# Optimization experiments

Hardware: AMD Instinct MI355X
Metric: run time of the kernel (lower is better)

## Reference

```python
import jax, jax.numpy as jnp
import numpy as np

EPS = 1e-12  # matches torch.nn.functional.normalize default eps

def _l2_normalize(x):
    # F.normalize: x / max(||x||_2, eps)
    n = jnp.linalg.norm(x, axis=-1, keepdims=True)
    return x / jnp.maximum(n, EPS)

def setup_inputs() -> dict:
    key = jax.random.key(0)
    k_z, k_e = jax.random.split(key)
    B, N, D, K = 8, 4096, 64, 8192
    z = jax.random.normal(k_z, (B, N, D), dtype=jnp.float32)
    # nn.Embedding weight initialized uniform(-1/K, 1/K)
    embedding = jax.random.uniform(k_e, (K, D), dtype=jnp.float32,
                                   minval=-1.0 / K, maxval=1.0 / K)
    return {"z": z, "embedding": embedding, "temperature": 1.0}

def reference(z, embedding, temperature):
    z_norm = _l2_normalize(z)                      # (B,N,D)
    codebook = _l2_normalize(embedding)            # (K,D)
    sim = jnp.einsum('bnd,kd->bnk', z_norm, codebook)  # (B,N,K)
    dists = 1.0 - sim
    probs = jax.nn.softmax(-dists / temperature, axis=-1)  # (B,N,K)
    z_q = jnp.einsum('bnk,kd->bnd', probs, codebook)       # (B,N,D)
    return (probs, z_q)
```

## Files before the change

### kernel.cpp

```cpp
#include <hip/hip_runtime.h>


#define M_TOTAL 32768
#define KCODES  8192
#define DDIM    64
#define KSPLIT  4
#define KCHUNK  (KCODES / KSPLIT)
#define M_ROWS  128

typedef __attribute__((ext_vector_type(8))) short bf16x8;
typedef __attribute__((ext_vector_type(4))) short bf16x4;
typedef __attribute__((ext_vector_type(4))) float f32x4;

__device__ inline unsigned short f2bf(float x) {
  union { float f; unsigned u; } v; v.f = x;
  unsigned r = v.u + 0x7FFFu + ((v.u >> 16) & 1u);
  return (unsigned short)(r >> 16);
}

__global__ __launch_bounds__(256) void norm_rows_kernel(
    const float* __restrict__ in, unsigned short* __restrict__ F,
    unsigned short* __restrict__ FT, int nrows) {
  int row = blockIdx.x * 4 + (threadIdx.x >> 6);
  int d = threadIdx.x & 63;
  if (row >= nrows) return;
  float x = in[(size_t)row * DDIM + d];
  float s = x * x;
  s += __shfl_xor(s, 1);  s += __shfl_xor(s, 2);  s += __shfl_xor(s, 4);
  s += __shfl_xor(s, 8);  s += __shfl_xor(s, 16); s += __shfl_xor(s, 32);
  float scale = 1.0f / fmaxf(sqrtf(s), 1e-12f);
  unsigned short b = f2bf(x * scale);
  {
    int blk = row >> 4, ml = row & 15;
    int h = d >> 5, g = (d >> 3) & 3, j = d & 7;
    F[((size_t)(blk * 2 + h)) * 512 + (g * 16 + ml) * 8 + j] = b;
  }
  if (FT) {
    int ds = d >> 4, dl = d & 15;
    int kb = row >> 5, kg = (row >> 3) & 3, kj = row & 7;
    FT[((size_t)(kb * 4 + ds)) * 512 + (kg * 16 + dl) * 8 + kj] = b;
  }
}

__global__ __launch_bounds__(512, 4) void passA_kernel(
    const unsigned short* __restrict__ FZn,
    const unsigned short* __restrict__ FCb,
    const unsigned short* __restrict__ FCbT,
    const float* __restrict__ tptr,
    float* __restrict__ Up,
    float* __restrict__ rsp) {
  __shared__ __align__(16) unsigned short sbuf[2][4096];
  __shared__ __align__(16) unsigned short etile[8][16 * 56];
  const int tid = threadIdx.x;
  const int w  = tid >> 6, l = tid & 63, g = l >> 4, ml = l & 15;
  const int rb = blockIdx.x & 255;
  const int ks = blockIdx.x >> 8;
  const int m_base = rb * M_ROWS + w * 16;
  const int k0 = ks * KCHUNK;
  const float sc = 1.4426950408889634f / tptr[0];

  const unsigned short* fz = FZn + ((size_t)((rb * 8 + w) * 2)) * 512;
  const bf16x8 zn0 = *(const bf16x8*)(fz + l * 8);
  const bf16x8 zn1 = *(const bf16x8*)(fz + 512 + l * 8);

  const f32x4 zero = {0.f, 0.f, 0.f, 0.f};
  f32x4 uacc[4] = {zero, zero, zero, zero};
  float rs = 0.f;

  const unsigned short* gb = (tid < 256 ? FCb : FCbT) + (size_t)(tid & 255) * 8;
  bf16x8 stg = *(const bf16x8*)(gb + (size_t)k0 * 64);
  int cur = 0;

  const int NIT = KCHUNK / 32;
  for (int it = 0; it < NIT; ++it) {
    *(bf16x8*)&sbuf[cur][tid * 8] = stg;
    if (it + 1 < NIT)
      stg = *(const bf16x8*)(gb + (size_t)(k0 + (it + 1) * 32) * 64);
    __syncthreads();
    const unsigned short* sb = &sbuf[cur][0];
#pragma unroll
    for (int cs = 0; cs < 2; ++cs) {
      const bf16x8 cb0 = *(const bf16x8*)(sb + (cs * 2 + 0) * 512 + l * 8);
      const bf16x8 cb1 = *(const bf16x8*)(sb + (cs * 2 + 1) * 512 + l * 8);
      f32x4 acc = __builtin_amdgcn_mfma_f32_16x16x32_bf16(cb0, zn0, zero, 0, 0, 0);
      acc = __builtin_amdgcn_mfma_f32_16x16x32_bf16(cb1, zn1, acc, 0, 0, 0);
      bf16x4 ep;
#pragma unroll
      for (int r = 0; r < 4; ++r) {
        float e = exp2f((acc[r] - 1.0f) * sc);
        rs += e;
        ep[r] = (short)f2bf(e);
      }
      *(bf16x4*)&etile[w][ml * 56 + cs * 16 + g * 4] = ep;
    }
    asm volatile("s_waitcnt lgkmcnt(0)" ::: "memory");
    const bf16x8 ef = *(const bf16x8*)&etile[w][ml * 56 + g * 8];
#pragma unroll
    for (int ds = 0; ds < 4; ++ds) {
      const bf16x8 ct = *(const bf16x8*)(sb + 2048 + ds * 512 + l * 8);
      uacc[ds] = __builtin_amdgcn_mfma_f32_16x16x32_bf16(ct, ef, uacc[ds], 0, 0, 0);
    }
    cur ^= 1;
  }

  rs += __shfl_xor(rs, 16);
  rs += __shfl_xor(rs, 32);
  if (g == 0) rsp[(size_t)ks * M_TOTAL + m_base + ml] = rs;

  float* urow = Up + ((size_t)ks * M_TOTAL + m_base + ml) * DDIM;
#pragma unroll
  for (int ds = 0; ds < 4; ++ds)
    *(f32x4*)(urow + ds * 16 + g * 4) = uacc[ds];
}

__global__ __launch_bounds__(256) void rs_kernel(
    const float* __restrict__ rsp, float* __restrict__ rs) {
  int m = blockIdx.x * 256 + threadIdx.x;
  float s = 0.f;
#pragma unroll
  for (int ks = 0; ks < KSPLIT; ++ks) s += rsp[(size_t)ks * M_TOTAL + m];
  rs[m] = s;
}

__global__ __launch_bounds__(256) void zq_kernel(
    const float* __restrict__ Up, const float* __restrict__ rs,
    float* __restrict__ zq) {
  size_t i = (size_t)blockIdx.x * 256 + threadIdx.x;
  f32x4 u = *(const f32x4*)(Up + i * 4);
#pragma unroll
  for (int ks = 1; ks < KSPLIT; ++ks) {
    f32x4 p = *(const f32x4*)(Up + (size_t)ks * M_TOTAL * DDIM + i * 4);
#pragma unroll
    for (int r = 0; r < 4; ++r) u[r] += p[r];
  }
  float inv = 1.0f / rs[(i * 4) >> 6];
  f32x4 v = {u[0] * inv, u[1] * inv, u[2] * inv, u[3] * inv};
  *(f32x4*)(zq + i * 4) = v;
}

__global__ __launch_bounds__(512, 4) void probs_kernel(
    const unsigned short* __restrict__ FZn,
    const unsigned short* __restrict__ FCb,
    const float* __restrict__ tptr,
    const float* __restrict__ rsv,
    float* __restrict__ probs) {
  __shared__ __align__(16) unsigned short sbuf[2][4096];
  const int tid = threadIdx.x;
  const int w  = tid >> 6, l = tid & 63, g = l >> 4, ml = l & 15;
  const int rb = blockIdx.x & 255;
  const int ks = blockIdx.x >> 8;
  const int m_base = rb * M_ROWS + w * 16;
  const int k0 = ks * KCHUNK;
  const float sc = 1.4426950408889634f / tptr[0];

  const unsigned short* fz = FZn + ((size_t)((rb * 8 + w) * 2)) * 512;
  const bf16x8 zn0 = *(const bf16x8*)(fz + l * 8);
  const bf16x8 zn1 = *(const bf16x8*)(fz + 512 + l * 8);
  const float inv = 1.0f / rsv[m_base + ml];
  const f32x4 zero = {0.f, 0.f, 0.f, 0.f};
  float* prow = probs + (size_t)(m_base + ml) * KCODES;

  const unsigned short* gb = FCb + (size_t)tid * 8;
  bf16x8 stg = *(const bf16x8*)(gb + (size_t)k0 * 64);
  int cur = 0;

  const int NIT = KCHUNK / 64;
  for (int it = 0; it < NIT; ++it) {
    *(bf16x8*)&sbuf[cur][tid * 8] = stg;
    if (it + 1 < NIT)
      stg = *(const bf16x8*)(gb + (size_t)(k0 + (it + 1) * 64) * 64);
    __syncthreads();
    const unsigned short* sb = &sbuf[cur][0];
    const int kc = k0 + it * 64;
#pragma unroll
    for (int cb = 0; cb < 4; ++cb) {
      const bf16x8 c0 = *(const bf16x8*)(sb + (cb * 2 + 0) * 512 + l * 8);
      const bf16x8 c1 = *(const bf16x8*)(sb + (cb * 2 + 1) * 512 + l * 8);
      f32x4 a = __builtin_amdgcn_mfma_f32_16x16x32_bf16(c0, zn0, zero, 0, 0, 0);
      a = __builtin_amdgcn_mfma_f32_16x16x32_bf16(c1, zn1, a, 0, 0, 0);
      f32x4 p;
#pragma unroll
      for (int r = 0; r < 4; ++r) p[r] = exp2f((a[r] - 1.0f) * sc) * inv;
      *(f32x4*)(prow + kc + cb * 16 + g * 4) = p;
    }
    cur ^= 1;
  }
}

extern "C" void kernel_launch(void* const* d_in, const int* in_sizes, int n_in,
                              void* d_out, int out_size, void* d_ws, size_t ws_size,
                              hipStream_t stream) {
  const float* z    = (const float*)d_in[0];
  const float* emb  = (const float*)d_in[1];
  const float* temp = (const float*)d_in[2];

  float* probs = (float*)d_out;
  float* zq    = probs + (size_t)M_TOTAL * KCODES;

  unsigned short* FZn  = (unsigned short*)d_ws;
  unsigned short* FCb  = FZn + (size_t)M_TOTAL * DDIM;
  unsigned short* FCbT = FCb + (size_t)KCODES * DDIM;
  float* Up  = (float*)(FCbT + (size_t)KCODES * DDIM);
  float* rsp = Up + (size_t)KSPLIT * M_TOTAL * DDIM;
  float* rs  = rsp + (size_t)KSPLIT * M_TOTAL;

  norm_rows_kernel<<<M_TOTAL / 4, 256, 0, stream>>>(z, FZn, nullptr, M_TOTAL);
  norm_rows_kernel<<<KCODES / 4, 256, 0, stream>>>(emb, FCb, FCbT, KCODES);
  passA_kernel<<<256 * KSPLIT, 512, 0, stream>>>(FZn, FCb, FCbT, temp, Up, rsp);
  rs_kernel<<<M_TOTAL / 256, 256, 0, stream>>>(rsp, rs);
  zq_kernel<<<(M_TOTAL * DDIM / 4) / 256, 256, 0, stream>>>(Up, rs, zq);
  probs_kernel<<<256 * KSPLIT, 512, 0, stream>>>(FZn, FCb, temp, rs, probs);
}
```

Measured before the change: 378.1 us.

## Drop LDS staging of codebook, read from global; shrink blocks; fuse rs/zq kernels

The pass-A and probs kernels no longer stage codebook tiles through double-buffered shared memory with block barriers. Each wave now reads codebook fragments directly from global memory (relying on L2/L1 caching), and blocks shrink from 512 to 256 threads with twice as many blocks. The row-sum reduction is folded into the z_q normalization kernel, which removes one launch. bf16 packing now uses the HIP intrinsic conversion. The trade-off is more redundant global/cache traffic per wave in exchange for removing barriers and LDS pressure.

```diff
diff --git a/kernel.cpp b/kernel.cpp
--- a/kernel.cpp
+++ b/kernel.cpp
@@ -1,4 +1,5 @@
 #include <hip/hip_runtime.h>
+#include <hip/hip_bf16.h>
 
 
 #define M_TOTAL 32768
@@ -6,10 +7,8 @@
 #define DDIM    64
 #define KSPLIT  4
 #define KCHUNK  (KCODES / KSPLIT)
-#define M_ROWS  128
 
 typedef __attribute__((ext_vector_type(8))) short bf16x8;
-typedef __attribute__((ext_vector_type(4))) short bf16x4;
 typedef __attribute__((ext_vector_type(4))) float f32x4;
 
 __device__ inline unsigned short f2bf(float x) {
@@ -42,24 +41,23 @@
   }
 }
 
-__global__ __launch_bounds__(512, 4) void passA_kernel(
+__global__ __launch_bounds__(256) void passA_kernel(
     const unsigned short* __restrict__ FZn,
     const unsigned short* __restrict__ FCb,
     const unsigned short* __restrict__ FCbT,
     const float* __restrict__ tptr,
     float* __restrict__ Up,
     float* __restrict__ rsp) {
-  __shared__ __align__(16) unsigned short sbuf[2][4096];
-  __shared__ __align__(16) unsigned short etile[8][16 * 56];
+  __shared__ __align__(16) unsigned short etile[4][16 * 56];
   const int tid = threadIdx.x;
   const int w  = tid >> 6, l = tid & 63, g = l >> 4, ml = l & 15;
-  const int rb = blockIdx.x & 255;
-  const int ks = blockIdx.x >> 8;
-  const int m_base = rb * M_ROWS + w * 16;
+  const int rb = blockIdx.x & 511;
+  const int ks = blockIdx.x >> 9;
+  const int m_base = rb * 64 + w * 16;
   const int k0 = ks * KCHUNK;
   const float sc = 1.4426950408889634f / tptr[0];
 
-  const unsigned short* fz = FZn + ((size_t)((rb * 8 + w) * 2)) * 512;
+  const unsigned short* fz = FZn + ((size_t)((rb * 4 + w) * 2)) * 512;
   const bf16x8 zn0 = *(const bf16x8*)(fz + l * 8);
   const bf16x8 zn1 = *(const bf16x8*)(fz + 512 + l * 8);
 
@@ -67,40 +65,32 @@
   f32x4 uacc[4] = {zero, zero, zero, zero};
   float rs = 0.f;
 
-  const unsigned short* gb = (tid < 256 ? FCb : FCbT) + (size_t)(tid & 255) * 8;
-  bf16x8 stg = *(const bf16x8*)(gb + (size_t)k0 * 64);
-  int cur = 0;
-
-  const int NIT = KCHUNK / 32;
-  for (int it = 0; it < NIT; ++it) {
-    *(bf16x8*)&sbuf[cur][tid * 8] = stg;
-    if (it + 1 < NIT)
-      stg = *(const bf16x8*)(gb + (size_t)(k0 + (it + 1) * 32) * 64);
-    __syncthreads();
-    const unsigned short* sb = &sbuf[cur][0];
+  for (int kc = k0; kc < k0 + KCHUNK; kc += 32) {
+    const unsigned short* fc = FCb + (size_t)(kc >> 4) * 1024;
+    const unsigned short* ft = FCbT + (size_t)(kc >> 5) * 2048;
 #pragma unroll
     for (int cs = 0; cs < 2; ++cs) {
-      const bf16x8 cb0 = *(const bf16x8*)(sb + (cs * 2 + 0) * 512 + l * 8);
-      const bf16x8 cb1 = *(const bf16x8*)(sb + (cs * 2 + 1) * 512 + l * 8);
-      f32x4 acc = __builtin_amdgcn_mfma_f32_16x16x32_bf16(cb0, zn0, zero, 0, 0, 0);
-      acc = __builtin_amdgcn_mfma_f32_16x16x32_bf16(cb1, zn1, acc, 0, 0, 0);
-      bf16x4 ep;
-#pragma unroll
-      for (int r = 0; r < 4; ++r) {
-        float e = exp2f((acc[r] - 1.0f) * sc);
-        rs += e;
-        ep[r] = (short)f2bf(e);
-      }
-      *(bf16x4*)&etile[w][ml * 56 + cs * 16 + g * 4] = ep;
+      const bf16x8 c0 = *(const bf16x8*)(fc + cs * 1024 + l * 8);
+      const bf16x8 c1 = *(const bf16x8*)(fc + cs * 1024 + 512 + l * 8);
+      f32x4 acc = __builtin_amdgcn_mfma_f32_16x16x32_bf16(c0, zn0, zero, 0, 0, 0);
+      acc = __builtin_amdgcn_mfma_f32_16x16x32_bf16(c1, zn1, acc, 0, 0, 0);
+      float e0 = exp2f((acc[0] - 1.0f) * sc);
+      float e1 = exp2f((acc[1] - 1.0f) * sc);
+      float e2 = exp2f((acc[2] - 1.0f) * sc);
+      float e3 = exp2f((acc[3] - 1.0f) * sc);
+      rs += (e0 + e1) + (e2 + e3);
+      union { __hip_bfloat162 h[2]; uint2 u; } pk;
+      pk.h[0] = __float22bfloat162_rn(make_float2(e0, e1));
+      pk.h[1] = __float22bfloat162_rn(make_float2(e2, e3));
+      *(uint2*)&etile[w][ml * 56 + cs * 16 + g * 4] = pk.u;
     }
     asm volatile("s_waitcnt lgkmcnt(0)" ::: "memory");
     const bf16x8 ef = *(const bf16x8*)&etile[w][ml * 56 + g * 8];
 #pragma unroll
     for (int ds = 0; ds < 4; ++ds) {
-      const bf16x8 ct = *(const bf16x8*)(sb + 2048 + ds * 512 + l * 8);
+      const bf16x8 ct = *(const bf16x8*)(ft + ds * 512 + l * 8);
       uacc[ds] = __builtin_amdgcn_mfma_f32_16x16x32_bf16(ct, ef, uacc[ds], 0, 0, 0);
     }
-    cur ^= 1;
   }
 
   rs += __shfl_xor(rs, 16);
@@ -113,19 +103,13 @@
     *(f32x4*)(urow + ds * 16 + g * 4) = uacc[ds];
 }
 
-__global__ __launch_bounds__(256) void rs_kernel(
-    const float* __restrict__ rsp, float* __restrict__ rs) {
-  int m = blockIdx.x * 256 + threadIdx.x;
-  float s = 0.f;
-#pragma unroll
-  for (int ks = 0; ks < KSPLIT; ++ks) s += rsp[(size_t)ks * M_TOTAL + m];
-  rs[m] = s;
-}
-
-__global__ __launch_bounds__(256) void zq_kernel(
-    const float* __restrict__ Up, const float* __restrict__ rs,
-    float* __restrict__ zq) {
+__global__ __launch_bounds__(256) void rszq_kernel(
+    const float* __restrict__ Up, const float* __restrict__ rsp,
+    float* __restrict__ rs, float* __restrict__ zq) {
   size_t i = (size_t)blockIdx.x * 256 + threadIdx.x;
+  int m = (int)(i >> 4);
+  float s = rsp[m] + rsp[M_TOTAL + m] + rsp[2 * M_TOTAL + m] + rsp[3 * M_TOTAL + m];
+  if ((i & 15) == 0) rs[m] = s;
   f32x4 u = *(const f32x4*)(Up + i * 4);
 #pragma unroll
   for (int ks = 1; ks < KSPLIT; ++ks) {
@@ -133,57 +117,45 @@
 #pragma unroll
     for (int r = 0; r < 4; ++r) u[r] += p[r];
   }
-  float inv = 1.0f / rs[(i * 4) >> 6];
+  float inv = 1.0f / s;
   f32x4 v = {u[0] * inv, u[1] * inv, u[2] * inv, u[3] * inv};
   *(f32x4*)(zq + i * 4) = v;
 }
 
-__global__ __launch_bounds__(512, 4) void probs_kernel(
+__global__ __launch_bounds__(256) void probs_kernel(
     const unsigned short* __restrict__ FZn,
     const unsigned short* __restrict__ FCb,
     const float* __restrict__ tptr,
     const float* __restrict__ rsv,
     float* __restrict__ probs) {
-  __shared__ __align__(16) unsigned short sbuf[2][4096];
   const int tid = threadIdx.x;
   const int w  = tid >> 6, l = tid & 63, g = l >> 4, ml = l & 15;
-  const int rb = blockIdx.x & 255;
-  const int ks = blockIdx.x >> 8;
-  const int m_base = rb * M_ROWS + w * 16;
+  const int rb = blockIdx.x & 511;
+  const int ks = blockIdx.x >> 9;
+  const int m_base = rb * 64 + w * 16;
   const int k0 = ks * KCHUNK;
   const float sc = 1.4426950408889634f / tptr[0];
 
-  const unsigned short* fz = FZn + ((size_t)((rb * 8 + w) * 2)) * 512;
+  const unsigned short* fz = FZn + ((size_t)((rb * 4 + w) * 2)) * 512;
   const bf16x8 zn0 = *(const bf16x8*)(fz + l * 8);
   const bf16x8 zn1 = *(const bf16x8*)(fz + 512 + l * 8);
   const float inv = 1.0f / rsv[m_base + ml];
   const f32x4 zero = {0.f, 0.f, 0.f, 0.f};
   float* prow = probs + (size_t)(m_base + ml) * KCODES;
 
-  const unsigned short* gb = FCb + (size_t)tid * 8;
-  bf16x8 stg = *(const bf16x8*)(gb + (size_t)k0 * 64);
-  int cur = 0;
-
-  const int NIT = KCHUNK / 64;
-  for (int it = 0; it < NIT; ++it) {
-    *(bf16x8*)&sbuf[cur][tid * 8] = stg;
-    if (it + 1 < NIT)
-      stg = *(const bf16x8*)(gb + (size_t)(k0 + (it + 1) * 64) * 64);
-    __syncthreads();
-    const unsigned short* sb = &sbuf[cur][0];
-    const int kc = k0 + it * 64;
+  for (int kc = k0; kc < k0 + KCHUNK; kc += 32) {
+    const unsigned short* fc = FCb + (size_t)(kc >> 4) * 1024;
 #pragma unroll
-    for (int cb = 0; cb < 4; ++cb) {
-      const bf16x8 c0 = *(const bf16x8*)(sb + (cb * 2 + 0) * 512 + l * 8);
-      const bf16x8 c1 = *(const bf16x8*)(sb + (cb * 2 + 1) * 512 + l * 8);
+    for (int cs = 0; cs < 2; ++cs) {
+      const bf16x8 c0 = *(const bf16x8*)(fc + cs * 1024 + l * 8);
+      const bf16x8 c1 = *(const bf16x8*)(fc + cs * 1024 + 512 + l * 8);
       f32x4 a = __builtin_amdgcn_mfma_f32_16x16x32_bf16(c0, zn0, zero, 0, 0, 0);
       a = __builtin_amdgcn_mfma_f32_16x16x32_bf16(c1, zn1, a, 0, 0, 0);
       f32x4 p;
 #pragma unroll
       for (int r = 0; r < 4; ++r) p[r] = exp2f((a[r] - 1.0f) * sc) * inv;
-      *(f32x4*)(prow + kc + cb * 16 + g * 4) = p;
+      *(f32x4*)(prow + kc + cs * 16 + g * 4) = p;
     }
-    cur ^= 1;
   }
 }
 
@@ -206,8 +178,7 @@
 
   norm_rows_kernel<<<M_TOTAL / 4, 256, 0, stream>>>(z, FZn, nullptr, M_TOTAL);
   norm_rows_kernel<<<KCODES / 4, 256, 0, stream>>>(emb, FCb, FCbT, KCODES);
-  passA_kernel<<<256 * KSPLIT, 512, 0, stream>>>(FZn, FCb, FCbT, temp, Up, rsp);
-  rs_kernel<<<M_TOTAL / 256, 256, 0, stream>>>(rsp, rs);
-  zq_kernel<<<(M_TOTAL * DDIM / 4) / 256, 256, 0, stream>>>(Up, rs, zq);
-  probs_kernel<<<256 * KSPLIT, 512, 0, stream>>>(FZn, FCb, temp, rs, probs);
+  passA_kernel<<<512 * KSPLIT, 256, 0, stream>>>(FZn, FCb, FCbT, temp, Up, rsp);
+  rszq_kernel<<<(M_TOTAL * DDIM / 4) / 256, 256, 0, stream>>>(Up, rsp, rs, zq);
+  probs_kernel<<<512 * KSPLIT, 256, 0, stream>>>(FZn, FCb, temp, rs, probs);
 }
```

After: 502.0 us. 1.33x slower.

## Process two row tiles per wave in passA and fuse rowsum into zq kernel

Applied to the files above, without the earlier changes.

Each wave in passA now handles 32 rows (two 16-row tiles) instead of 16, so every codebook fragment loaded from shared memory feeds twice as many MFMAs. The grid shrinks to 512 blocks. The rs_kernel and zq_kernel are merged into one kernel that sums the split rowsum partials inline, removing a launch and a round trip through rs. The bf16 packing now uses the packed hip_bf16 conversions. The cost is higher register pressure and fewer blocks in passA, which may hurt occupancy and load balance.

```diff
diff --git a/kernel.cpp b/kernel.cpp
--- a/kernel.cpp
+++ b/kernel.cpp
@@ -1,4 +1,5 @@
 #include <hip/hip_runtime.h>
+#include <hip/hip_bf16.h>
 
 
 #define M_TOTAL 32768
@@ -6,10 +7,8 @@
 #define DDIM    64
 #define KSPLIT  4
 #define KCHUNK  (KCODES / KSPLIT)
-#define M_ROWS  128
 
 typedef __attribute__((ext_vector_type(8))) short bf16x8;
-typedef __attribute__((ext_vector_type(4))) short bf16x4;
 typedef __attribute__((ext_vector_type(4))) float f32x4;
 
 __device__ inline unsigned short f2bf(float x) {
@@ -50,22 +49,26 @@
     float* __restrict__ Up,
     float* __restrict__ rsp) {
   __shared__ __align__(16) unsigned short sbuf[2][4096];
-  __shared__ __align__(16) unsigned short etile[8][16 * 56];
+  __shared__ __align__(16) unsigned short etile[8][2][16 * 56];
   const int tid = threadIdx.x;
   const int w  = tid >> 6, l = tid & 63, g = l >> 4, ml = l & 15;
-  const int rb = blockIdx.x & 255;
-  const int ks = blockIdx.x >> 8;
-  const int m_base = rb * M_ROWS + w * 16;
+  const int rb = blockIdx.x & 127;
+  const int ks = blockIdx.x >> 7;
+  const int mA = rb * 256 + w * 32;
+  const int mB = mA + 16;
   const int k0 = ks * KCHUNK;
   const float sc = 1.4426950408889634f / tptr[0];
 
-  const unsigned short* fz = FZn + ((size_t)((rb * 8 + w) * 2)) * 512;
-  const bf16x8 zn0 = *(const bf16x8*)(fz + l * 8);
-  const bf16x8 zn1 = *(const bf16x8*)(fz + 512 + l * 8);
+  const unsigned short* fz = FZn + ((size_t)((rb * 16 + w * 2) * 2)) * 512;
+  const bf16x8 zA0 = *(const bf16x8*)(fz + l * 8);
+  const bf16x8 zA1 = *(const bf16x8*)(fz + 512 + l * 8);
+  const bf16x8 zB0 = *(const bf16x8*)(fz + 1024 + l * 8);
+  const bf16x8 zB1 = *(const bf16x8*)(fz + 1536 + l * 8);
 
   const f32x4 zero = {0.f, 0.f, 0.f, 0.f};
-  f32x4 uacc[4] = {zero, zero, zero, zero};
-  float rs = 0.f;
+  f32x4 uaccA[4] = {zero, zero, zero, zero};
+  f32x4 uaccB[4] = {zero, zero, zero, zero};
+  float rsA = 0.f, rsB = 0.f;
 
   const unsigned short* gb = (tid < 256 ? FCb : FCbT) + (size_t)(tid & 255) * 8;
   bf16x8 stg = *(const bf16x8*)(gb + (size_t)k0 * 64);
@@ -80,52 +83,61 @@
     const unsigned short* sb = &sbuf[cur][0];
 #pragma unroll
     for (int cs = 0; cs < 2; ++cs) {
-      const bf16x8 cb0 = *(const bf16x8*)(sb + (cs * 2 + 0) * 512 + l * 8);
-      const bf16x8 cb1 = *(const bf16x8*)(sb + (cs * 2 + 1) * 512 + l * 8);
-      f32x4 acc = __builtin_amdgcn_mfma_f32_16x16x32_bf16(cb0, zn0, zero, 0, 0, 0);
-      acc = __builtin_amdgcn_mfma_f32_16x16x32_bf16(cb1, zn1, acc, 0, 0, 0);
-      bf16x4 ep;
-#pragma unroll
-      for (int r = 0; r < 4; ++r) {
-        float e = exp2f((acc[r] - 1.0f) * sc);
-        rs += e;
-        ep[r] = (short)f2bf(e);
-      }
-      *(bf16x4*)&etile[w][ml * 56 + cs * 16 + g * 4] = ep;
+      const bf16x8 c0 = *(const bf16x8*)(sb + cs * 1024 + l * 8);
+      const bf16x8 c1 = *(const bf16x8*)(sb + cs * 1024 + 512 + l * 8);
+      f32x4 aA = __builtin_amdgcn_mfma_f32_16x16x32_bf16(c0, zA0, zero, 0, 0, 0);
+      aA = __builtin_amdgcn_mfma_f32_16x16x32_bf16(c1, zA1, aA, 0, 0, 0);
+      f32x4 aB = __builtin_amdgcn_mfma_f32_16x16x32_bf16(c0, zB0, zero, 0, 0, 0);
+      aB = __builtin_amdgcn_mfma_f32_16x16x32_bf16(c1, zB1, aB, 0, 0, 0);
+      float eA0 = exp2f((aA[0] - 1.0f) * sc), eA1 = exp2f((aA[1] - 1.0f) * sc);
+      float eA2 = exp2f((aA[2] - 1.0f) * sc), eA3 = exp2f((aA[3] - 1.0f) * sc);
+      float eB0 = exp2f((aB[0] - 1.0f) * sc), eB1 = exp2f((aB[1] - 1.0f) * sc);
+      float eB2 = exp2f((aB[2] - 1.0f) * sc), eB3 = exp2f((aB[3] - 1.0f) * sc);
+      rsA += (eA0 + eA1) + (eA2 + eA3);
+      rsB += (eB0 + eB1) + (eB2 + eB3);
+      union { __hip_bfloat162 h[2]; uint2 u; } pA, pB;
+      pA.h[0] = __float22bfloat162_rn(make_float2(eA0, eA1));
+      pA.h[1] = __float22bfloat162_rn(make_float2(eA2, eA3));
+      pB.h[0] = __float22bfloat162_rn(make_float2(eB0, eB1));
+      pB.h[1] = __float22bfloat162_rn(make_float2(eB2, eB3));
+      *(uint2*)&etile[w][0][ml * 56 + cs * 16 + g * 4] = pA.u;
+      *(uint2*)&etile[w][1][ml * 56 + cs * 16 + g * 4] = pB.u;
     }
     asm volatile("s_waitcnt lgkmcnt(0)" ::: "memory");
-    const bf16x8 ef = *(const bf16x8*)&etile[w][ml * 56 + g * 8];
+    const bf16x8 efA = *(const bf16x8*)&etile[w][0][ml * 56 + g * 8];
+    const bf16x8 efB = *(const bf16x8*)&etile[w][1][ml * 56 + g * 8];
 #pragma unroll
     for (int ds = 0; ds < 4; ++ds) {
       const bf16x8 ct = *(const bf16x8*)(sb + 2048 + ds * 512 + l * 8);
-      uacc[ds] = __builtin_amdgcn_mfma_f32_16x16x32_bf16(ct, ef, uacc[ds], 0, 0, 0);
+      uaccA[ds] = __builtin_amdgcn_mfma_f32_16x16x32_bf16(ct, efA, uaccA[ds], 0, 0, 0);
+      uaccB[ds] = __builtin_amdgcn_mfma_f32_16x16x32_bf16(ct, efB, uaccB[ds], 0, 0, 0);
     }
     cur ^= 1;
   }
 
-  rs += __shfl_xor(rs, 16);
-  rs += __shfl_xor(rs, 32);
-  if (g == 0) rsp[(size_t)ks * M_TOTAL + m_base + ml] = rs;
-
-  float* urow = Up + ((size_t)ks * M_TOTAL + m_base + ml) * DDIM;
-#pragma unroll
-  for (int ds = 0; ds < 4; ++ds)
-    *(f32x4*)(urow + ds * 16 + g * 4) = uacc[ds];
-}
-
-__global__ __launch_bounds__(256) void rs_kernel(
-    const float* __restrict__ rsp, float* __restrict__ rs) {
-  int m = blockIdx.x * 256 + threadIdx.x;
-  float s = 0.f;
-#pragma unroll
-  for (int ks = 0; ks < KSPLIT; ++ks) s += rsp[(size_t)ks * M_TOTAL + m];
-  rs[m] = s;
-}
-
-__global__ __launch_bounds__(256) void zq_kernel(
-    const float* __restrict__ Up, const float* __restrict__ rs,
-    float* __restrict__ zq) {
+  rsA += __shfl_xor(rsA, 16);  rsA += __shfl_xor(rsA, 32);
+  rsB += __shfl_xor(rsB, 16);  rsB += __shfl_xor(rsB, 32);
+  if (g == 0) {
+    rsp[(size_t)ks * M_TOTAL + mA + ml] = rsA;
+    rsp[(size_t)ks * M_TOTAL + mB + ml] = rsB;
+  }
+
+  float* urA = Up + ((size_t)ks * M_TOTAL + mA + ml) * DDIM;
+  float* urB = Up + ((size_t)ks * M_TOTAL + mB + ml) * DDIM;
+#pragma unroll
+  for (int ds = 0; ds < 4; ++ds) {
+    *(f32x4*)(urA + ds * 16 + g * 4) = uaccA[ds];
+    *(f32x4*)(urB + ds * 16 + g * 4) = uaccB[ds];
+  }
+}
+
+__global__ __launch_bounds__(256) void rszq_kernel(
+    const float* __restrict__ Up, const float* __restrict__ rsp,
+    float* __restrict__ rs, float* __restrict__ zq) {
   size_t i = (size_t)blockIdx.x * 256 + threadIdx.x;
+  int m = (int)(i >> 4);
+  float s = rsp[m] + rsp[M_TOTAL + m] + rsp[2 * M_TOTAL + m] + rsp[3 * M_TOTAL + m];
+  if ((i & 15) == 0) rs[m] = s;
   f32x4 u = *(const f32x4*)(Up + i * 4);
 #pragma unroll
   for (int ks = 1; ks < KSPLIT; ++ks) {
@@ -133,7 +145,7 @@
 #pragma unroll
     for (int r = 0; r < 4; ++r) u[r] += p[r];
   }
-  float inv = 1.0f / rs[(i * 4) >> 6];
+  float inv = 1.0f / s;
   f32x4 v = {u[0] * inv, u[1] * inv, u[2] * inv, u[3] * inv};
   *(f32x4*)(zq + i * 4) = v;
 }
@@ -149,7 +161,7 @@
   const int w  = tid >> 6, l = tid & 63, g = l >> 4, ml = l & 15;
   const int rb = blockIdx.x & 255;
   const int ks = blockIdx.x >> 8;
-  const int m_base = rb * M_ROWS + w * 16;
+  const int m_base = rb * 128 + w * 16;
   const int k0 = ks * KCHUNK;
   const float sc = 1.4426950408889634f / tptr[0];
 
@@ -206,8 +218,7 @@
 
   norm_rows_kernel<<<M_TOTAL / 4, 256, 0, stream>>>(z, FZn, nullptr, M_TOTAL);
   norm_rows_kernel<<<KCODES / 4, 256, 0, stream>>>(emb, FCb, FCbT, KCODES);
-  passA_kernel<<<256 * KSPLIT, 512, 0, stream>>>(FZn, FCb, FCbT, temp, Up, rsp);
-  rs_kernel<<<M_TOTAL / 256, 256, 0, stream>>>(rsp, rs);
-  zq_kernel<<<(M_TOTAL * DDIM / 4) / 256, 256, 0, stream>>>(Up, rs, zq);
+  passA_kernel<<<128 * KSPLIT, 512, 0, stream>>>(FZn, FCb, FCbT, temp, Up, rsp);
+  rszq_kernel<<<(M_TOTAL * DDIM / 4) / 256, 256, 0, stream>>>(Up, rsp, rs, zq);
   probs_kernel<<<256 * KSPLIT, 512, 0, stream>>>(FZn, FCb, temp, rs, probs);
 }
```

Measured after the change: 378.6 us. No clear change (+0.1%).
